# Optimization experiments

Hardware: AMD Instinct MI355X
Metric: run time of the kernel (lower is better)

## Reference

```python
import jax, jax.numpy as jnp
import numpy as np
import math

B, T, C = 4, 2048, 1024
H, DQK, DV = 16, 64, 64

def setup_inputs() -> dict:
    key = jax.random.key(0)
    k1, k2, k3, k4, k5 = jax.random.split(key, 5)
    # randw(*d) = randn(*d) / sqrt(d[-1])
    x_q = jax.random.normal(k1, (B, T, C), dtype=jnp.float32)
    w_q = jax.random.normal(k2, (H, DQK, C), dtype=jnp.float32) / math.sqrt(C)
    w_k = jax.random.normal(k3, (H, DQK, C), dtype=jnp.float32) / math.sqrt(C)
    w_v = jax.random.normal(k4, (H, DV, C), dtype=jnp.float32) / math.sqrt(C)
    w_o = jax.random.normal(k5, (DV * H, C), dtype=jnp.float32) / math.sqrt(C)
    return {"x_q": x_q, "w_q": w_q, "w_k": w_k, "w_v": w_v, "w_o": w_o}

def reference(x_q, w_q, w_k, w_v, w_o):
    # self-attention: x_kv = x_q
    q = jnp.einsum('ntc,hdc->nhtd', x_q, w_q)
    k = jnp.einsum('ntc,hdc->nhtd', x_q, w_k)
    v = jnp.einsum('ntc,hdc->nhtd', x_q, w_v)
    a = jnp.einsum('nhtd,nhsd->nhts', q, k) / math.sqrt(q.shape[3])
    t = a.shape[2]
    causal_forbidden = jnp.arange(t)[:, None] < jnp.arange(t)[None, :]  # [T,S]
    a = jnp.where(causal_forbidden[None, None], -jnp.inf, a)
    a = jax.nn.softmax(a, axis=3)
    y = jnp.einsum('nhts,nhsd->nthd', a, v).reshape(a.shape[0], t, -1)
    return y @ w_o
```

## Files before the change

### kernel.cpp

```cpp
#include <hip/hip_runtime.h>
#include <stdint.h>

#define B_ 4
#define T_ 2048
#define C_ 1024
#define H_ 16
#define D_ 64
#define M_ (B_*T_)
#define K_ C_

typedef unsigned short ushort_t;
typedef __bf16 bf16x8 __attribute__((ext_vector_type(8)));
typedef float  float4_ __attribute__((ext_vector_type(4)));
typedef ushort_t ushort4_ __attribute__((ext_vector_type(4)));
typedef uint32_t uint32x2 __attribute__((ext_vector_type(2)));

__device__ __forceinline__ ushort_t f2bf(float f) {
    union { float f; uint32_t u; } c; c.f = f;
    uint32_t u = c.u;
    uint32_t r = (u + 0x7FFFu + ((u >> 16) & 1u)) >> 16;
    return (ushort_t)r;
}
__device__ __forceinline__ float4_ f4zero() { float4_ z; z[0]=0.f; z[1]=0.f; z[2]=0.f; z[3]=0.f; return z; }

__device__ __forceinline__ uint32_t cvtpk(float a, float b) {
    uint32_t r;
    asm("v_cvt_pk_bf16_f32 %0, %1, %2" : "=v"(r) : "v"(a), "v"(b));
    return r;
}

#define GLDS16(gptr, lptr) \
    __builtin_amdgcn_global_load_lds((const __attribute__((address_space(1))) uint32_t*)(gptr), \
                                     (__attribute__((address_space(3))) uint32_t*)(lptr), 16, 0, 0)

__global__ __launch_bounds__(256) void prep_all(const float* __restrict__ x,
                                                ushort_t* __restrict__ x_bf,
                                                const float* __restrict__ s0,
                                                const float* __restrict__ s1,
                                                const float* __restrict__ s2,
                                                ushort_t* __restrict__ dst,
                                                const float* __restrict__ wo,
                                                ushort_t* __restrict__ wot) {
    __shared__ ushort_t tile[64][65];
    const int b = blockIdx.x;
    const int tid = threadIdx.x;
    if (b < 8192) {
        const int i = b * 1024 + tid * 4;
        float4_ v = *(const float4_*)(x + i);
        ushort4_ o;
        #pragma unroll
        for (int e = 0; e < 4; e++) o[e] = f2bf(v[e]);
        *(ushort4_*)(x_bf + i) = o;
    } else if (b < 11264) {
        const int bw = b - 8192;
        const float* src = (bw < 1024) ? s0 : (bw < 2048) ? s1 : s2;
        const int off = (bw & 1023) * 1024 + tid * 4;
        float4_ v = *(const float4_*)(src + off);
        ushort4_ o;
        #pragma unroll
        for (int e = 0; e < 4; e++) o[e] = f2bf(v[e]);
        *(ushort4_*)(dst + (size_t)bw * 1024 + tid * 4) = o;
    } else {
        const int bb = b - 11264;
        const int c0 = (bb & 15) * 64;
        const int r0 = (bb >> 4) * 64;
        const int row = tid >> 2;
        const int col = (tid & 3) * 16;
        #pragma unroll
        for (int r = 0; r < 4; r++) {
            float4_ v = *(const float4_*)(wo + (size_t)(r0 + row) * 1024 + c0 + col + r * 4);
            #pragma unroll
            for (int e = 0; e < 4; e++) tile[row][col + r * 4 + e] = f2bf(v[e]);
        }
        __syncthreads();
        #pragma unroll
        for (int r = 0; r < 2; r++) {
            bf16x8 v;
            #pragma unroll
            for (int e = 0; e < 8; e++) v[e] = __builtin_bit_cast(__bf16, tile[col + r * 8 + e][row]);
            *(bf16x8*)(wot + (size_t)(c0 + row) * 1024 + r0 + col + r * 8) = v;
        }
    }
}

template<int MODE>
__global__ __launch_bounds__(256, 4)
void gemm_bt(const ushort_t* __restrict__ A,
             const ushort_t* __restrict__ Bt,
             ushort_t* __restrict__ q_ws, ushort_t* __restrict__ k_ws,
             ushort_t* __restrict__ vt_ws, float* __restrict__ outp)
{
    __shared__ __align__(16) ushort_t As[128 * 32];
    __shared__ __align__(16) ushort_t Bs[128 * 32];
    const int tid = threadIdx.x;
    const int NB   = gridDim.x * gridDim.y;
    const int flat = blockIdx.y * gridDim.x + blockIdx.x;
    const int fl2  = (flat & 7) * (NB >> 3) + (flat >> 3);
    const int m0 = (fl2 & 63) * 128;
    const int n0 = (fl2 >> 6) * 128;

    const int L    = tid & 63;
    const int wid  = tid >> 6;
    const int wr   = (wid >> 1) * 64;
    const int wc   = (wid & 1) * 64;
    const int quad = L >> 4;
    const int lc   = L & 15;

    float4_ acc[4][4];
    #pragma unroll
    for (int i = 0; i < 4; i++)
        #pragma unroll
        for (int j = 0; j < 4; j++) acc[i][j] = f4zero();

    const int loff0 = wid * 1024 + L * 16;
    for (int k0 = 0; k0 < K_; k0 += 32) {
        __syncthreads();
        #pragma unroll
        for (int r = 0; r < 2; r++) {
            const int off = loff0 + r * 4096;
            const int row = off >> 6;
            const int col = off & 63;
            const char* ga = (const char*)A  + (size_t)(m0 + row) * (K_ * 2) + k0 * 2 + col;
            const char* gb = (const char*)Bt + (size_t)(n0 + row) * (K_ * 2) + k0 * 2 + col;
            GLDS16(ga, (char*)As + off);
            GLDS16(gb, (char*)Bs + off);
        }
        __syncthreads();
        bf16x8 af[4], bfr[4];
        #pragma unroll
        for (int i = 0; i < 4; i++) {
            const int m = wr + i * 16 + lc;
            af[i]  = *(const bf16x8*)((const char*)As + m * 64 + quad * 16);
            const int n = wc + i * 16 + lc;
            bfr[i] = *(const bf16x8*)((const char*)Bs + n * 64 + quad * 16);
        }
        #pragma unroll
        for (int i = 0; i < 4; i++)
            #pragma unroll
            for (int j = 0; j < 4; j++)
                acc[i][j] = __builtin_amdgcn_mfma_f32_16x16x32_bf16(af[i], bfr[j], acc[i][j], 0, 0, 0);
    }

    const int mat = n0 >> 10;
    const int nb  = n0 & 1023;
    if (MODE == 1) {
        #pragma unroll
        for (int i = 0; i < 4; i++)
            #pragma unroll
            for (int j = 0; j < 4; j++)
                #pragma unroll
                for (int rg = 0; rg < 4; rg++) {
                    const int mg = m0 + wr + i * 16 + quad * 4 + rg;
                    const int cg = n0 + wc + j * 16 + lc;
                    outp[(size_t)mg * 1024 + cg] = acc[i][j][rg];
                }
    } else if (mat == 2) {
        #pragma unroll
        for (int i = 0; i < 4; i++) {
            const int mg0 = m0 + wr + i * 16 + quad * 4;
            const int n = mg0 >> 11, t0 = mg0 & 2047;
            #pragma unroll
            for (int j = 0; j < 4; j++) {
                const int ln = nb + wc + j * 16 + lc;
                const int h = ln >> 6, d = ln & 63;
                const int nh = n * H_ + h;
                ushort4_ pk;
                #pragma unroll
                for (int rg = 0; rg < 4; rg++) pk[rg] = f2bf(acc[i][j][rg]);
                *(ushort4_*)(vt_ws + ((size_t)nh * 64 + d) * T_ + t0) = pk;
            }
        }
    } else {
        const float scl = (mat == 0) ? 0.18033688011112042f : 1.0f;
        ushort_t* dstp  = (mat == 0) ? q_ws : k_ws;
        #pragma unroll
        for (int i = 0; i < 4; i++)
            #pragma unroll
            for (int j = 0; j < 4; j++)
                #pragma unroll
                for (int rg = 0; rg < 4; rg++) {
                    const int mg = m0 + wr + i * 16 + quad * 4 + rg;
                    const int ln = nb + wc + j * 16 + lc;
                    const int h = ln >> 6, d = ln & 63;
                    const int n = mg >> 11, t = mg & 2047;
                    const int nh = n * H_ + h;
                    dstp[((size_t)nh * T_ + t) * 64 + d] = f2bf(acc[i][j][rg] * scl);
                }
    }
}

#define KP 72

__global__ __launch_bounds__(512)
void attn(const ushort_t* __restrict__ q_ws, const ushort_t* __restrict__ k_ws,
          const ushort_t* __restrict__ vt_ws, ushort_t* __restrict__ y_ws)
{
    __shared__ __align__(16) ushort_t Ks[2][64 * 64];
    __shared__ __align__(16) ushort_t Vs[2][64 * 64];
    __shared__ __align__(16) ushort_t Ps[8][16 * KP];
    const int tid  = threadIdx.x;
    const int L    = tid & 63;
    const int w    = tid >> 6;
    const int quad = L >> 4, lc = L & 15;
    const int bid  = blockIdx.x;
    const int qt   = 15 - (bid >> 6);
    const int nh   = bid & 63;
    const int n    = nh >> 4;
    const int tq0  = qt * 128 + w * 16;
    const int tg   = tq0 + lc;
    const int nt   = 2 * qt + 2;
    const int dstile = tq0 >> 6;

    const ushort_t* qbase = q_ws + ((size_t)nh * T_ + tq0) * 64;
    const bf16x8 qf0 = *(const bf16x8*)(qbase + (size_t)lc * 64 + quad * 8);
    const bf16x8 qf1 = *(const bf16x8*)(qbase + (size_t)lc * 64 + quad * 8 + 32);

    float m_i = -1e30f, l_i = 0.f;
    float4_ o[4];
    #pragma unroll
    for (int r = 0; r < 4; r++) o[r] = f4zero();

    const char* kbase = (const char*)(k_ws  + (size_t)nh * T_ * 64);
    const char* vbase = (const char*)(vt_ws + (size_t)nh * 64 * T_);
    char* pwr = (char*)Ps[w] + lc * (KP * 2);

    const int ldsoff = tid * 16;
    const int srow   = ldsoff >> 7;
    const int sslot  = (ldsoff >> 4) & 7;
    const int sgs    = sslot ^ (srow & 7);
    const size_t kgo = (size_t)srow * 128 + sgs * 16;
    const size_t vgo = (size_t)srow * (T_ * 2) + sgs * 16;

    int off16[4][2];
    #pragma unroll
    for (int b = 0; b < 4; b++) {
        const int row = b * 16 + lc;
        const int r7  = lc & 7;
        off16[b][0] = row * 128 + ((quad ^ r7) << 4);
        off16[b][1] = row * 128 + (((quad + 4) ^ r7) << 4);
    }

    auto STAGE = [&](int st, int b) {
        GLDS16(kbase + (size_t)st * 8192 + kgo, (char*)Ks[b] + ldsoff);
        GLDS16(vbase + (size_t)st * 128  + vgo, (char*)Vs[b] + ldsoff);
    };

    STAGE(0, 0);
    __syncthreads();
    int cur = 0;

    for (int st = 0; st < nt; st++) {
        if (st + 1 < nt) STAGE(st + 1, cur ^ 1);
        if (st * 64 <= tq0 + 15) {
            const char* ks = (const char*)Ks[cur];
            const char* vs = (const char*)Vs[cur];

            float4_ s[4];
            #pragma unroll
            for (int sb = 0; sb < 4; sb++) {
                const bf16x8 kf0 = *(const bf16x8*)(ks + off16[sb][0]);
                const bf16x8 kf1 = *(const bf16x8*)(ks + off16[sb][1]);
                float4_ a = f4zero();
                a = __builtin_amdgcn_mfma_f32_16x16x32_bf16(kf0, qf0, a, 0, 0, 0);
                a = __builtin_amdgcn_mfma_f32_16x16x32_bf16(kf1, qf1, a, 0, 0, 0);
                s[sb] = a;
            }
            if (st >= dstile) {
                #pragma unroll
                for (int sb = 0; sb < 4; sb++)
                    #pragma unroll
                    for (int rg = 0; rg < 4; rg++) {
                        const int sg = st * 64 + sb * 16 + quad * 4 + rg;
                        if (sg > tg) s[sb][rg] = -1e30f;
                    }
            }
            float rm = -1e30f;
            #pragma unroll
            for (int sb = 0; sb < 4; sb++)
                #pragma unroll
                for (int rg = 0; rg < 4; rg++) rm = fmaxf(rm, s[sb][rg]);
            rm = fmaxf(rm, __shfl_xor(rm, 16));
            rm = fmaxf(rm, __shfl_xor(rm, 32));
            if (!__all(rm <= m_i + 8.f)) {
                const float mn    = fmaxf(m_i, rm);
                const float alpha = __builtin_amdgcn_exp2f(m_i - mn);
                l_i *= alpha;
                #pragma unroll
                for (int db = 0; db < 4; db++)
                    #pragma unroll
                    for (int rg = 0; rg < 4; rg++) o[db][rg] *= alpha;
                m_i = mn;
            }
            float rs = 0.f;
            #pragma unroll
            for (int sb = 0; sb < 4; sb++)
                #pragma unroll
                for (int rg = 0; rg < 4; rg++) {
                    const float p = __builtin_amdgcn_exp2f(s[sb][rg] - m_i);
                    s[sb][rg] = p;
                    rs += p;
                }
            rs += __shfl_xor(rs, 16);
            rs += __shfl_xor(rs, 32);
            l_i += rs;

            #pragma unroll
            for (int sb = 0; sb < 4; sb++) {
                uint32x2 pk2;
                pk2[0] = cvtpk(s[sb][0], s[sb][1]);
                pk2[1] = cvtpk(s[sb][2], s[sb][3]);
                *(uint32x2*)(pwr + sb * 32 + quad * 8) = pk2;
            }

            const bf16x8 pa0 = *(const bf16x8*)(pwr + quad * 16);
            const bf16x8 pa1 = *(const bf16x8*)(pwr + 64 + quad * 16);
            #pragma unroll
            for (int db = 0; db < 4; db++) {
                const bf16x8 vf0 = *(const bf16x8*)(vs + off16[db][0]);
                const bf16x8 vf1 = *(const bf16x8*)(vs + off16[db][1]);
                o[db] = __builtin_amdgcn_mfma_f32_16x16x32_bf16(vf0, pa0, o[db], 0, 0, 0);
                o[db] = __builtin_amdgcn_mfma_f32_16x16x32_bf16(vf1, pa1, o[db], 0, 0, 0);
            }
        }
        __syncthreads();
        cur ^= 1;
    }

    const int h = nh & 15;
    const float inv = 1.f / l_i;
    ushort_t* yrow = y_ws + ((size_t)(n * T_ + tg)) * 1024 + h * 64;
    #pragma unroll
    for (int db = 0; db < 4; db++) {
        uint32x2 pk2;
        pk2[0] = cvtpk(o[db][0] * inv, o[db][1] * inv);
        pk2[1] = cvtpk(o[db][2] * inv, o[db][3] * inv);
        *(uint32x2*)(yrow + db * 16 + quad * 4) = pk2;
    }
}

extern "C" void kernel_launch(void* const* d_in, const int* in_sizes, int n_in,
                              void* d_out, int out_size, void* d_ws, size_t ws_size,
                              hipStream_t stream) {
    (void)in_sizes; (void)n_in; (void)out_size; (void)ws_size;
    const float* x  = (const float*)d_in[0];
    const float* wq = (const float*)d_in[1];
    const float* wk = (const float*)d_in[2];
    const float* wv = (const float*)d_in[3];
    const float* wo = (const float*)d_in[4];
    char* ws = (char*)d_ws;
    const size_t MB = (size_t)1024 * 1024;
    ushort_t* x_bf  = (ushort_t*)(ws);
    ushort_t* q_ws  = (ushort_t*)(ws + 16 * MB);
    ushort_t* k_ws  = (ushort_t*)(ws + 32 * MB);
    ushort_t* vt_ws = (ushort_t*)(ws + 48 * MB);
    ushort_t* wcat  = (ushort_t*)(ws + 64 * MB);
    ushort_t* wot   = (ushort_t*)(ws + 70 * MB);
    ushort_t* y_ws  = x_bf;
    float*    outp  = (float*)d_out;

    prep_all<<<dim3(11520), dim3(256), 0, stream>>>(x, x_bf, wq, wk, wv, wcat, wo, wot);
    gemm_bt<0><<<dim3(64, 24), dim3(256), 0, stream>>>(x_bf, wcat, q_ws, k_ws, vt_ws, nullptr);
    attn<<<dim3(1024), dim3(512), 0, stream>>>(q_ws, k_ws, vt_ws, y_ws);
    gemm_bt<1><<<dim3(64, 8), dim3(256), 0, stream>>>(y_ws, wot, nullptr, nullptr, nullptr, outp);
}
```

Baseline: 256.0 us.

## Double GEMM K-tile to 64 with XOR-swizzled LDS layout

```diff
diff --git a/kernel.cpp b/kernel.cpp
--- a/kernel.cpp
+++ b/kernel.cpp
@@ -84,20 +84,17 @@
 }
 
 template<int MODE>
-__global__ __launch_bounds__(256, 4)
+__global__ __launch_bounds__(256)
 void gemm_bt(const ushort_t* __restrict__ A,
              const ushort_t* __restrict__ Bt,
              ushort_t* __restrict__ q_ws, ushort_t* __restrict__ k_ws,
              ushort_t* __restrict__ vt_ws, float* __restrict__ outp)
 {
-    __shared__ __align__(16) ushort_t As[128 * 32];
-    __shared__ __align__(16) ushort_t Bs[128 * 32];
+    __shared__ __align__(16) ushort_t As[128 * 64];
+    __shared__ __align__(16) ushort_t Bs[128 * 64];
     const int tid = threadIdx.x;
-    const int NB   = gridDim.x * gridDim.y;
-    const int flat = blockIdx.y * gridDim.x + blockIdx.x;
-    const int fl2  = (flat & 7) * (NB >> 3) + (flat >> 3);
-    const int m0 = (fl2 & 63) * 128;
-    const int n0 = (fl2 >> 6) * 128;
+    const int m0 = blockIdx.x * 128;
+    const int n0 = blockIdx.y * 128;
 
     const int L    = tid & 63;
     const int wid  = tid >> 6;
@@ -112,33 +109,52 @@
         #pragma unroll
         for (int j = 0; j < 4; j++) acc[i][j] = f4zero();
 
-    const int loff0 = wid * 1024 + L * 16;
-    for (int k0 = 0; k0 < K_; k0 += 32) {
+    int l_off[4]; size_t a_off[4], b_off[4];
+    #pragma unroll
+    for (int r = 0; r < 4; r++) {
+        const int off = tid * 16 + r * 4096;
+        const int row = off >> 7;
+        const int sg  = ((off >> 4) & 7) ^ (row & 7);
+        l_off[r] = off;
+        a_off[r] = (size_t)(m0 + row) * 2048 + sg * 16;
+        b_off[r] = (size_t)(n0 + row) * 2048 + sg * 16;
+    }
+    const char* Ag = (const char*)A;
+    const char* Bg = (const char*)Bt;
+
+    int offA[4][2], offB[4][2];
+    #pragma unroll
+    for (int i = 0; i < 4; i++)
+        #pragma unroll
+        for (int ks = 0; ks < 2; ks++) {
+            const int ra = wr + i * 16 + lc;
+            const int rb = wc + i * 16 + lc;
+            offA[i][ks] = ra * 128 + (((ks * 4 + quad) ^ (lc & 7)) << 4);
+            offB[i][ks] = rb * 128 + (((ks * 4 + quad) ^ (lc & 7)) << 4);
+        }
+
+    for (int k0 = 0; k0 < K_; k0 += 64) {
         __syncthreads();
         #pragma unroll
-        for (int r = 0; r < 2; r++) {
-            const int off = loff0 + r * 4096;
-            const int row = off >> 6;
-            const int col = off & 63;
-            const char* ga = (const char*)A  + (size_t)(m0 + row) * (K_ * 2) + k0 * 2 + col;
-            const char* gb = (const char*)Bt + (size_t)(n0 + row) * (K_ * 2) + k0 * 2 + col;
-            GLDS16(ga, (char*)As + off);
-            GLDS16(gb, (char*)Bs + off);
+        for (int r = 0; r < 4; r++) {
+            GLDS16(Ag + a_off[r] + (size_t)k0 * 2, (char*)As + l_off[r]);
+            GLDS16(Bg + b_off[r] + (size_t)k0 * 2, (char*)Bs + l_off[r]);
         }
         __syncthreads();
-        bf16x8 af[4], bfr[4];
-        #pragma unroll
-        for (int i = 0; i < 4; i++) {
-            const int m = wr + i * 16 + lc;
-            af[i]  = *(const bf16x8*)((const char*)As + m * 64 + quad * 16);
-            const int n = wc + i * 16 + lc;
-            bfr[i] = *(const bf16x8*)((const char*)Bs + n * 64 + quad * 16);
-        }
-        #pragma unroll
-        for (int i = 0; i < 4; i++)
-            #pragma unroll
-            for (int j = 0; j < 4; j++)
-                acc[i][j] = __builtin_amdgcn_mfma_f32_16x16x32_bf16(af[i], bfr[j], acc[i][j], 0, 0, 0);
+        #pragma unroll
+        for (int ks = 0; ks < 2; ks++) {
+            bf16x8 af[4], bfr[4];
+            #pragma unroll
+            for (int i = 0; i < 4; i++) {
+                af[i]  = *(const bf16x8*)((const char*)As + offA[i][ks]);
+                bfr[i] = *(const bf16x8*)((const char*)Bs + offB[i][ks]);
+            }
+            #pragma unroll
+            for (int i = 0; i < 4; i++)
+                #pragma unroll
+                for (int j = 0; j < 4; j++)
+                    acc[i][j] = __builtin_amdgcn_mfma_f32_16x16x32_bf16(af[i], bfr[j], acc[i][j], 0, 0, 0);
+        }
     }
 
     const int mat = n0 >> 10;
```

Result: no change. 253.4 us (-1.0%).
